# Performance work log

Measured on AMD Instinct MI355X. Metric: run time of the kernel, lower is better.

## Reference

```python
import jax, jax.numpy as jnp
import numpy as np
from jax import lax

B, T, H, K = 64, 512, 768, 13


def setup_inputs() -> dict:
    key = jax.random.key(0)
    ks = jax.random.split(key, 6)
    hidden_states = jax.random.normal(ks[0], (B, T, H), dtype=jnp.float32)
    labels = jax.random.randint(ks[1], (B, T), 0, K, dtype=jnp.int64)
    attention_mask = jnp.ones((B, T), dtype=jnp.int32)  # torchcrf requires mask[:,0]=1
    W = jax.random.normal(ks[2], (H, K), dtype=jnp.float32) * 0.02
    b = jnp.zeros((K,), dtype=jnp.float32)
    start_transitions = jax.random.uniform(ks[3], (K,), minval=-0.1, maxval=0.1)
    end_transitions = jax.random.uniform(ks[4], (K,), minval=-0.1, maxval=0.1)
    transitions = jax.random.uniform(ks[5], (K, K), minval=-0.1, maxval=0.1)
    return {"hidden_states": hidden_states, "labels": labels,
            "attention_mask": attention_mask, "W": W, "b": b,
            "start_transitions": start_transitions,
            "end_transitions": end_transitions, "transitions": transitions}


def _crf_llh(emissions, tags, mask, start, end, trans):
    # emissions [B,T,K], tags [B,T] int, mask [B,T] bool
    Bn = emissions.shape[0]
    bidx = jnp.arange(Bn)
    maskf = mask.astype(emissions.dtype)

    # ---- numerator: score of the given tag sequence (vectorized gathers) ----
    tag_em = jnp.take_along_axis(emissions, tags[..., None], axis=2)[..., 0]  # [B,T]
    trans_sc = trans[tags[:, :-1], tags[:, 1:]]                               # [B,T-1]
    numerator = (start[tags[:, 0]] + tag_em[:, 0]
                 + jnp.sum((trans_sc + tag_em[:, 1:]) * maskf[:, 1:], axis=1))
    seq_ends = jnp.sum(mask.astype(jnp.int32), axis=1) - 1
    numerator = numerator + end[tags[bidx, seq_ends]]

    # ---- denominator: log partition via forward algorithm (scan over T) ----
    alpha0 = start[None, :] + emissions[:, 0]  # [B,K]

    def step(alpha, xs):
        em_t, m_t = xs  # [B,K], [B]
        nxt = jax.nn.logsumexp(alpha[:, :, None] + trans[None] + em_t[:, None, :], axis=1)
        alpha = jnp.where(m_t[:, None], nxt, alpha)
        return alpha, None

    xs = (jnp.swapaxes(emissions[:, 1:], 0, 1), jnp.swapaxes(mask[:, 1:], 0, 1))
    alpha, _ = lax.scan(step, alpha0, xs)
    denominator = jax.nn.logsumexp(alpha + end[None, :], axis=1)

    return jnp.sum(numerator - denominator)  # torchcrf default reduction='sum'


def reference(hidden_states, labels, attention_mask, W, b,
              start_transitions, end_transitions, transitions):
    # dropout is identity in eval mode
    logits = jnp.einsum('bth,hk->btk', hidden_states, W) + b  # [B,T,K]
    mask = attention_mask.astype(bool)
    llh = _crf_llh(logits, labels, mask, start_transitions,
                   end_transitions, transitions)
    loss = -1.0 * llh
    return (loss, logits)
```

## Files before the change

### kernel.cpp

```cpp
#include <hip/hip_runtime.h>
#include <hip/hip_bf16.h>

#define LOG2E 1.4426950408889634f
#define LN2   0.69314718055994531f

typedef __attribute__((ext_vector_type(8))) short short8;
typedef __attribute__((ext_vector_type(4))) float f32x4;

__device__ __forceinline__ unsigned bfbits(__bf16 x) {
  return (unsigned)__builtin_bit_cast(unsigned short, x);
}
__device__ __forceinline__ unsigned cvt2bf(float a, float b) {
  return bfbits((__bf16)a) | (bfbits((__bf16)b) << 16);
}

__device__ __forceinline__ float lse13(const float (&x)[13]) {
  float m = fmaxf(fmaxf(fmaxf(fmaxf(x[0], x[1]), fmaxf(x[2], x[3])),
                        fmaxf(fmaxf(x[4], x[5]), fmaxf(x[6], x[7]))),
                  fmaxf(fmaxf(fmaxf(x[8], x[9]), fmaxf(x[10], x[11])), x[12]));
  float s = (((exp2f(x[0] - m) + exp2f(x[1] - m)) + (exp2f(x[2] - m) + exp2f(x[3] - m))) +
             ((exp2f(x[4] - m) + exp2f(x[5] - m)) + (exp2f(x[6] - m) + exp2f(x[7] - m)))) +
            (((exp2f(x[8] - m) + exp2f(x[9] - m)) + (exp2f(x[10] - m) + exp2f(x[11] - m))) +
             exp2f(x[12] - m));
  return m + log2f(s);
}

__global__ __launch_bounds__(64) void k0_packW(const float* __restrict__ W,
                                               uint4* __restrict__ pwsHi,
                                               uint4* __restrict__ pwsLo,
                                               float* __restrict__ out0) {
  const int lane = threadIdx.x;
  const int g = lane >> 4;
  const int n = lane & 15;
  for (int kk = 0; kk < 24; ++kk) {
    unsigned hw[4], lw[4];
#pragma unroll
    for (int p = 0; p < 4; ++p) {
      const int h0 = kk * 32 + g * 8 + 2 * p;
      float v0 = (n < 13) ? W[h0 * 13 + n] : 0.0f;
      float v1 = (n < 13) ? W[(h0 + 1) * 13 + n] : 0.0f;
      __bf16 b0 = (__bf16)v0, b1 = (__bf16)v1;
      float r0 = v0 - (float)b0, r1 = v1 - (float)b1;
      hw[p] = bfbits(b0) | (bfbits(b1) << 16);
      lw[p] = cvt2bf(r0, r1);
    }
    pwsHi[kk * 64 + lane] = make_uint4(hw[0], hw[1], hw[2], hw[3]);
    pwsLo[kk * 64 + lane] = make_uint4(lw[0], lw[1], lw[2], lw[3]);
  }
  if (lane == 0) out0[0] = 0.0f;
}

__global__ __launch_bounds__(64) void k1_logits_mfma(const float* __restrict__ hs,
                                                     const uint4* __restrict__ pwsHi,
                                                     const uint4* __restrict__ pwsLo,
                                                     const float* __restrict__ bias,
                                                     float* __restrict__ logits) {
  const int lane = threadIdx.x;
  const int g = lane >> 4;
  const int n = lane & 15;

  const size_t row = (size_t)blockIdx.x * 16 + n;
  const float* ap = hs + row * 768 + g * 8;
  f32x4 acc = {0.0f, 0.0f, 0.0f, 0.0f};

#pragma unroll 6
  for (int kk = 0; kk < 24; ++kk) {
    const float4 a0 = *(const float4*)(ap + kk * 32);
    const float4 a1 = *(const float4*)(ap + kk * 32 + 4);
    const uint4 wh = pwsHi[kk * 64 + lane];
    const uint4 wl = pwsLo[kk * 64 + lane];
    float v[8] = {a0.x, a0.y, a0.z, a0.w, a1.x, a1.y, a1.z, a1.w};
    unsigned hw[4], lw[4];
#pragma unroll
    for (int p = 0; p < 4; ++p) {
      float x0 = v[2 * p], x1 = v[2 * p + 1];
      __bf16 b0 = (__bf16)x0, b1 = (__bf16)x1;
      float r0 = x0 - (float)b0, r1 = x1 - (float)b1;
      hw[p] = bfbits(b0) | (bfbits(b1) << 16);
      lw[p] = cvt2bf(r0, r1);
    }
    const short8 ahi = __builtin_bit_cast(short8, make_uint4(hw[0], hw[1], hw[2], hw[3]));
    const short8 alo = __builtin_bit_cast(short8, make_uint4(lw[0], lw[1], lw[2], lw[3]));
    const short8 bhi = __builtin_bit_cast(short8, wh);
    const short8 blo = __builtin_bit_cast(short8, wl);
    acc = __builtin_amdgcn_mfma_f32_16x16x32_bf16(ahi, bhi, acc, 0, 0, 0);
    acc = __builtin_amdgcn_mfma_f32_16x16x32_bf16(alo, bhi, acc, 0, 0, 0);
    acc = __builtin_amdgcn_mfma_f32_16x16x32_bf16(ahi, blo, acc, 0, 0, 0);
  }

  if (n < 13) {
    const float bj = bias[n];
#pragma unroll
    for (int r = 0; r < 4; ++r)
      logits[((size_t)blockIdx.x * 16 + g * 4 + r) * 13 + n] = acc[r] + bj;
  }
}

__global__ __launch_bounds__(64) void k2a_chunks(const float* __restrict__ logits,
                                                 const int* __restrict__ amask,
                                                 const float* __restrict__ trans,
                                                 float* __restrict__ wsQ) {
  const int bc = blockIdx.x;
  const int b = bc >> 5;
  const int c = bc & 31;
  const int t0 = 1 + (c << 4);
  const int nt = min(16, 512 - t0);
  const int tid = threadIdx.x;
  __shared__ float trs[13 * 14];
  __shared__ float ems[16 * 14];
  __shared__ int msk[16];
  __shared__ float P[2][13 * 20];

  for (int idx = tid; idx < 169; idx += 64) {
    int i = idx / 13;
    int jj = idx - i * 13;
    trs[i * 14 + jj] = trans[idx] * LOG2E;
  }
  for (int idx = tid; idx < nt * 13; idx += 64) {
    int ts = idx / 13;
    int jj = idx - ts * 13;
    ems[ts * 14 + jj] = logits[((size_t)(b << 9) + t0 + ts) * 13 + jj] * LOG2E;
  }
  if (tid < nt) msk[tid] = amask[(b << 9) + t0 + tid];
  __syncthreads();

  int cr[3], cj[3];
  bool cv[3];
#pragma unroll
  for (int s = 0; s < 3; ++s) {
    const int cell = tid + (s << 6);
    cv[s] = cell < 169;
    const int cc = cv[s] ? cell : 0;
    cr[s] = cc / 13;
    cj[s] = cc - cr[s] * 13;
  }
  float tr[3][13];
#pragma unroll
  for (int s = 0; s < 3; ++s)
#pragma unroll
    for (int i = 0; i < 13; ++i) tr[s][i] = trs[i * 14 + cj[s]];

  int cur = 0;
  bool inited = false;
  for (int ts = 0; ts < nt; ++ts) {
    if (msk[ts]) {
      if (!inited) {
#pragma unroll
        for (int s = 0; s < 3; ++s)
          if (cv[s]) P[cur][cr[s] * 20 + cj[s]] = trs[cr[s] * 14 + cj[s]] + ems[ts * 14 + cj[s]];
        inited = true;
      } else {
#pragma unroll
        for (int s = 0; s < 3; ++s) {
          if (cv[s]) {
            const float* pr = &P[cur][cr[s] * 20];
            float x[13];
#pragma unroll
            for (int i = 0; i < 13; ++i) x[i] = pr[i] + tr[s][i];
            P[cur ^ 1][cr[s] * 20 + cj[s]] = lse13(x) + ems[ts * 14 + cj[s]];
          }
        }
        cur ^= 1;
      }
    }
  }
#pragma unroll
  for (int s = 0; s < 3; ++s) {
    if (cv[s]) {
      float v;
      if (inited) v = P[cur][cr[s] * 20 + cj[s]];
      else v = (cr[s] == cj[s]) ? 0.0f : -1e30f;
      wsQ[(size_t)bc * 169 + tid + (s << 6)] = v;
    }
  }
}

__global__ __launch_bounds__(64) void k2b_combine(const float* __restrict__ logits,
                                                  const int* __restrict__ labels,
                                                  const int* __restrict__ amask,
                                                  const float* __restrict__ stt,
                                                  const float* __restrict__ endt,
                                                  const float* __restrict__ trans,
                                                  const float* __restrict__ wsQ,
                                                  float* __restrict__ out0) {
  const int b = blockIdx.x;
  const int lane = threadIdx.x;
  float contrib = 0.0f;
  int msum = 0;
#pragma unroll
  for (int it = 0; it < 8; ++it) {
    const int t = (it << 6) + lane;
    const int base = (b << 9) + t;
    const int tag = labels[base];
    const int mk = amask[base];
    msum += mk;
    const float em = logits[(size_t)base * 13 + tag];
    if (t == 0) contrib += stt[tag] + em;
    else if (mk) contrib += trans[labels[base - 1] * 13 + tag] + em;
  }
#pragma unroll
  for (int off = 32; off; off >>= 1) {
    contrib += __shfl_xor(contrib, off);
    msum += __shfl_xor(msum, off);
  }
  const float num = contrib + endt[labels[(b << 9) + msum - 1]];
  const int j = (lane < 13) ? lane : 0;
  float a = (stt[j] + logits[(size_t)(b << 9) * 13 + j]) * LOG2E;
  const float* Qb = wsQ + (size_t)b * (32 * 169);
  float q[13];
#pragma unroll
  for (int i = 0; i < 13; ++i) q[i] = Qb[i * 13 + j];
  for (int c = 0; c < 32; ++c) {
    float qn[13];
    if (c + 1 < 32) {
      const float* Qn = Qb + (c + 1) * 169;
#pragma unroll
      for (int i = 0; i < 13; ++i) qn[i] = Qn[i * 13 + j];
    }
    float x[13];
#pragma unroll
    for (int i = 0; i < 13; ++i) {
      const float ai = __int_as_float(__builtin_amdgcn_readlane(__float_as_int(a), i));
      x[i] = ai + q[i];
    }
    a = lse13(x);
#pragma unroll
    for (int i = 0; i < 13; ++i) q[i] = qn[i];
  }
  float z = (lane < 13) ? (a + endt[lane] * LOG2E) : -1e30f;
  float mz = z;
#pragma unroll
  for (int off = 32; off; off >>= 1) mz = fmaxf(mz, __shfl_xor(mz, off));
  float ez = exp2f(z - mz);
#pragma unroll
  for (int off = 32; off; off >>= 1) ez += __shfl_xor(ez, off);
  if (lane == 0) {
    const float llh = num - (mz + log2f(ez)) * LN2;
    atomicAdd(out0, -llh);
  }
}

extern "C" void kernel_launch(void* const* d_in, const int* in_sizes, int n_in,
                              void* d_out, int out_size, void* d_ws, size_t ws_size,
                              hipStream_t stream) {
  const float* hs = (const float*)d_in[0];
  const int* labels = (const int*)d_in[1];
  const int* amask = (const int*)d_in[2];
  const float* W = (const float*)d_in[3];
  const float* bias = (const float*)d_in[4];
  const float* stt = (const float*)d_in[5];
  const float* endt = (const float*)d_in[6];
  const float* trans = (const float*)d_in[7];

  float* out = (float*)d_out;
  float* logits = out + 1;

  uint4* pwsHi = (uint4*)d_ws;
  uint4* pwsLo = pwsHi + 24 * 64;
  float* wsQ = (float*)(pwsLo + 24 * 64);

  k0_packW<<<1, 64, 0, stream>>>(W, pwsHi, pwsLo, out);
  k1_logits_mfma<<<2048, 64, 0, stream>>>(hs, pwsHi, pwsLo, bias, logits);
  k2a_chunks<<<64 * 32, 64, 0, stream>>>(logits, amask, trans, wsQ);
  k2b_combine<<<64, 64, 0, stream>>>(logits, labels, amask, stt, endt, trans, wsQ, out);
}
```

Before: 229.1 us.

## Drop split-bf16 error compensation and software-pipeline loads in logits MFMA

```diff
diff --git a/kernel.cpp b/kernel.cpp
--- a/kernel.cpp
+++ b/kernel.cpp
@@ -26,33 +26,27 @@
 }
 
 __global__ __launch_bounds__(64) void k0_packW(const float* __restrict__ W,
-                                               uint4* __restrict__ pwsHi,
-                                               uint4* __restrict__ pwsLo,
+                                               uint4* __restrict__ pws,
                                                float* __restrict__ out0) {
   const int lane = threadIdx.x;
   const int g = lane >> 4;
   const int n = lane & 15;
   for (int kk = 0; kk < 24; ++kk) {
-    unsigned hw[4], lw[4];
+    unsigned hw[4];
 #pragma unroll
     for (int p = 0; p < 4; ++p) {
       const int h0 = kk * 32 + g * 8 + 2 * p;
       float v0 = (n < 13) ? W[h0 * 13 + n] : 0.0f;
       float v1 = (n < 13) ? W[(h0 + 1) * 13 + n] : 0.0f;
-      __bf16 b0 = (__bf16)v0, b1 = (__bf16)v1;
-      float r0 = v0 - (float)b0, r1 = v1 - (float)b1;
-      hw[p] = bfbits(b0) | (bfbits(b1) << 16);
-      lw[p] = cvt2bf(r0, r1);
-    }
-    pwsHi[kk * 64 + lane] = make_uint4(hw[0], hw[1], hw[2], hw[3]);
-    pwsLo[kk * 64 + lane] = make_uint4(lw[0], lw[1], lw[2], lw[3]);
+      hw[p] = cvt2bf(v0, v1);
+    }
+    pws[kk * 64 + lane] = make_uint4(hw[0], hw[1], hw[2], hw[3]);
   }
   if (lane == 0) out0[0] = 0.0f;
 }
 
 __global__ __launch_bounds__(64) void k1_logits_mfma(const float* __restrict__ hs,
-                                                     const uint4* __restrict__ pwsHi,
-                                                     const uint4* __restrict__ pwsLo,
+                                                     const uint4* __restrict__ pws,
                                                      const float* __restrict__ bias,
                                                      float* __restrict__ logits) {
   const int lane = threadIdx.x;
@@ -63,29 +57,32 @@
   const float* ap = hs + row * 768 + g * 8;
   f32x4 acc = {0.0f, 0.0f, 0.0f, 0.0f};
 
-#pragma unroll 6
+  float4 A0[4], A1[4];
+  uint4 Wv[4];
+#pragma unroll
+  for (int s = 0; s < 3; ++s) {
+    A0[s] = *(const float4*)(ap + s * 32);
+    A1[s] = *(const float4*)(ap + s * 32 + 4);
+    Wv[s] = pws[s * 64 + lane];
+  }
+
+#pragma unroll
   for (int kk = 0; kk < 24; ++kk) {
-    const float4 a0 = *(const float4*)(ap + kk * 32);
-    const float4 a1 = *(const float4*)(ap + kk * 32 + 4);
-    const uint4 wh = pwsHi[kk * 64 + lane];
-    const uint4 wl = pwsLo[kk * 64 + lane];
-    float v[8] = {a0.x, a0.y, a0.z, a0.w, a1.x, a1.y, a1.z, a1.w};
-    unsigned hw[4], lw[4];
-#pragma unroll
-    for (int p = 0; p < 4; ++p) {
-      float x0 = v[2 * p], x1 = v[2 * p + 1];
-      __bf16 b0 = (__bf16)x0, b1 = (__bf16)x1;
-      float r0 = x0 - (float)b0, r1 = x1 - (float)b1;
-      hw[p] = bfbits(b0) | (bfbits(b1) << 16);
-      lw[p] = cvt2bf(r0, r1);
-    }
-    const short8 ahi = __builtin_bit_cast(short8, make_uint4(hw[0], hw[1], hw[2], hw[3]));
-    const short8 alo = __builtin_bit_cast(short8, make_uint4(lw[0], lw[1], lw[2], lw[3]));
-    const short8 bhi = __builtin_bit_cast(short8, wh);
-    const short8 blo = __builtin_bit_cast(short8, wl);
-    acc = __builtin_amdgcn_mfma_f32_16x16x32_bf16(ahi, bhi, acc, 0, 0, 0);
-    acc = __builtin_amdgcn_mfma_f32_16x16x32_bf16(alo, bhi, acc, 0, 0, 0);
-    acc = __builtin_amdgcn_mfma_f32_16x16x32_bf16(ahi, blo, acc, 0, 0, 0);
+    const int cur = kk & 3;
+    const int nxt = (kk + 3) & 3;
+    if (kk + 3 < 24) {
+      A0[nxt] = *(const float4*)(ap + (kk + 3) * 32);
+      A1[nxt] = *(const float4*)(ap + (kk + 3) * 32 + 4);
+      Wv[nxt] = pws[(kk + 3) * 64 + lane];
+    }
+    unsigned hw[4];
+    hw[0] = cvt2bf(A0[cur].x, A0[cur].y);
+    hw[1] = cvt2bf(A0[cur].z, A0[cur].w);
+    hw[2] = cvt2bf(A1[cur].x, A1[cur].y);
+    hw[3] = cvt2bf(A1[cur].z, A1[cur].w);
+    const short8 a = __builtin_bit_cast(short8, make_uint4(hw[0], hw[1], hw[2], hw[3]));
+    const short8 b = __builtin_bit_cast(short8, Wv[cur]);
+    acc = __builtin_amdgcn_mfma_f32_16x16x32_bf16(a, b, acc, 0, 0, 0);
   }
 
   if (n < 13) {
@@ -255,12 +252,11 @@
   float* out = (float*)d_out;
   float* logits = out + 1;
 
-  uint4* pwsHi = (uint4*)d_ws;
-  uint4* pwsLo = pwsHi + 24 * 64;
-  float* wsQ = (float*)(pwsLo + 24 * 64);
-
-  k0_packW<<<1, 64, 0, stream>>>(W, pwsHi, pwsLo, out);
-  k1_logits_mfma<<<2048, 64, 0, stream>>>(hs, pwsHi, pwsLo, bias, logits);
+  uint4* pws = (uint4*)d_ws;
+  float* wsQ = (float*)(pws + 24 * 64);
+
+  k0_packW<<<1, 64, 0, stream>>>(W, pws, out);
+  k1_logits_mfma<<<2048, 64, 0, stream>>>(hs, pws, bias, logits);
   k2a_chunks<<<64 * 32, 64, 0, stream>>>(logits, amask, trans, wsQ);
   k2b_combine<<<64, 64, 0, stream>>>(logits, labels, amask, stt, endt, trans, wsQ, out);
 }
```

Result: slower. 272.9 us (+19.1%).
